# Kernel tuning notes

Hardware: AMD Instinct MI355X
Metric: run time of the kernel (lower is better)

## Reference

```python
import jax, jax.numpy as jnp
import numpy as np
import math

D_MODEL = 512
NHEAD = 8
N_LAYERS = 3
D_FF = 2048
INPUT_DIM = 128
NUM_CLASSES = 64
FACTOR = 5


def setup_inputs() -> dict:
    key = jax.random.key(0)
    ks = jax.random.split(key, 24)
    s = 0.02
    d, f, nl = D_MODEL, D_FF, N_LAYERS
    inp = {
        "x": jax.random.normal(ks[0], (4, 1024, INPUT_DIM), dtype=jnp.float32),
        "W_emb": jax.random.normal(ks[1], (INPUT_DIM, d), dtype=jnp.float32) * s,
        "b_emb": jnp.zeros((d,), jnp.float32),
        "Wq": jax.random.normal(ks[2], (nl, d, d), dtype=jnp.float32) * s,
        "bq": jnp.zeros((nl, d), jnp.float32),
        "Wk": jax.random.normal(ks[3], (nl, d, d), dtype=jnp.float32) * s,
        "bk": jnp.zeros((nl, d), jnp.float32),
        "Wv": jax.random.normal(ks[4], (nl, d, d), dtype=jnp.float32) * s,
        "bv": jnp.zeros((nl, d), jnp.float32),
        "Wo": jax.random.normal(ks[5], (nl, d, d), dtype=jnp.float32) * s,
        "bo": jnp.zeros((nl, d), jnp.float32),
        "ln1_g": jnp.ones((nl, d), jnp.float32),
        "ln1_b": jnp.zeros((nl, d), jnp.float32),
        "W1": jax.random.normal(ks[6], (nl, d, f), dtype=jnp.float32) * s,
        "b1": jnp.zeros((nl, f), jnp.float32),
        "W2": jax.random.normal(ks[7], (nl, f, d), dtype=jnp.float32) * s,
        "b2": jnp.zeros((nl, d), jnp.float32),
        "ln2_g": jnp.ones((nl, d), jnp.float32),
        "ln2_b": jnp.zeros((nl, d), jnp.float32),
        "W_dec": jax.random.normal(ks[8], (d, NUM_CLASSES), dtype=jnp.float32) * s,
        "b_dec": jnp.zeros((NUM_CLASSES,), jnp.float32),
    }
    return inp


def _layer_norm(x, g, b, eps=1e-5):
    m = jnp.mean(x, axis=-1, keepdims=True)
    v = jnp.var(x, axis=-1, keepdims=True)
    return (x - m) * jax.lax.rsqrt(v + eps) * g + b


def _pos_encoding(L, d):
    pos = jnp.arange(L, dtype=jnp.float32)[:, None]
    div = jnp.exp(jnp.arange(0, d, 2, dtype=jnp.float32) * (-math.log(10000.0) / d))
    pe = jnp.zeros((L, d), jnp.float32)
    pe = pe.at[:, 0::2].set(jnp.sin(pos * div))
    pe = pe.at[:, 1::2].set(jnp.cos(pos * div))
    return pe


def _prob_sparse_attn(x, Wq, bq, Wk, bk, Wv, bv, Wo, bo):
    B, L, d = x.shape
    H, dk = NHEAD, d // NHEAD
    u = min(L, int(FACTOR * math.log(L)) if L > 1 else L)
    Q = (x @ Wq + bq).reshape(B, L, H, dk).transpose(0, 2, 1, 3)  # bhld
    K = (x @ Wk + bk).reshape(B, L, H, dk).transpose(0, 2, 1, 3)
    V = (x @ Wv + bv).reshape(B, L, H, dk).transpose(0, 2, 1, 3)
    scores = jnp.einsum("bhld,bhmd->bhlm", Q, K) / math.sqrt(dk)  # [B,H,L,L]
    kth = jax.lax.top_k(scores, u)[0][..., -1:]  # kth-largest per row
    scores = jnp.where(scores < kth, -10000.0, scores)
    attn = jax.nn.softmax(scores, axis=-1)
    out = jnp.einsum("bhlm,bhmd->bhld", attn, V)
    out = out.transpose(0, 2, 1, 3).reshape(B, L, d)
    return out @ Wo + bo


def reference(x, W_emb, b_emb, Wq, bq, Wk, bk, Wv, bv, Wo, bo,
              ln1_g, ln1_b, W1, b1, W2, b2, ln2_g, ln2_b, W_dec, b_dec):
    B, L, _ = x.shape
    h = (x @ W_emb + b_emb) * math.sqrt(D_MODEL)
    h = h + _pos_encoding(L, D_MODEL)[None]
    for i in range(N_LAYERS):
        a = _prob_sparse_attn(h, Wq[i], bq[i], Wk[i], bk[i], Wv[i], bv[i], Wo[i], bo[i])
        h = _layer_norm(h + a, ln1_g[i], ln1_b[i])
        ff = jax.nn.relu(h @ W1[i] + b1[i]) @ W2[i] + b2[i]
        h = _layer_norm(h + ff, ln2_g[i], ln2_b[i])
    return h @ W_dec + b_dec
```

## Files before the change

kernel.cpp:

```cpp
#include <hip/hip_runtime.h>
#include <math.h>

#define SEQ 1024
#define BATCH 4
#define DMODEL 512
#define NHEAD 8
#define DK 64
#define DFF 2048
#define U_TOP 34
#define ROWS (BATCH * SEQ)

typedef unsigned short ushort_t;
typedef __attribute__((ext_vector_type(8))) short short8;
typedef __attribute__((ext_vector_type(4))) float float4v;

__device__ inline ushort_t f2bf(float f) {
  unsigned u = __float_as_uint(f);
  unsigned r = u + 0x7fffu + ((u >> 16) & 1u);
  return (ushort_t)(r >> 16);
}
__device__ inline float bf2f(ushort_t u) {
  return __uint_as_float((unsigned)u << 16);
}
__device__ inline float keyinv(unsigned cand) {
  unsigned fb = (cand & 0x80000000u) ? (cand ^ 0x80000000u) : ~cand;
  return __uint_as_float(fb);
}

__device__ inline void glds16(const void* g, void* l) {
  __builtin_amdgcn_global_load_lds(
      (const __attribute__((address_space(1))) unsigned int*)g,
      (__attribute__((address_space(3))) unsigned int*)l, 16, 0, 0);
}

__device__ inline float bitonic64_desc(float sv, int lane) {
#pragma unroll
  for (int k = 2; k <= 64; k <<= 1) {
#pragma unroll
    for (int j = k >> 1; j > 0; j >>= 1) {
      float pv = __shfl_xor(sv, j);
      bool keepMin = (((lane & k) != 0) == ((lane & j) == 0));
      sv = keepMin ? fminf(sv, pv) : fmaxf(sv, pv);
    }
  }
  return sv;
}

template <int RELU, int SPLIT>
__global__ __launch_bounds__(256) void gemm128(
    const ushort_t* __restrict__ A, const short* __restrict__ Bt,
    const float* __restrict__ b0, const float* __restrict__ b1,
    const float* __restrict__ b2, ushort_t* __restrict__ Cout,
    int K, int N, int zCstride) {
  __shared__ short As[128 * 32];
  __shared__ short Bs[128 * 32];

  const int tid = threadIdx.x;
  const int lane = tid & 63, w = tid >> 6;
  const int wm = w >> 1, wn = w & 1;
  const int quad = lane >> 4, r16 = lane & 15;
  const int bm = blockIdx.y * 128, bn = blockIdx.x * 128;

  const int srow = lane >> 2, skseg = lane & 3;
  const ushort_t* Ag0 = A + (size_t)(bm + w * 16 + srow) * K + skseg * 8;
  const ushort_t* Ag1 = Ag0 + (size_t)64 * K;
  const short* Bg0 = Bt + (size_t)(bn + w * 16 + srow) * K + skseg * 8;
  const short* Bg1 = Bg0 + (size_t)64 * K;
  short* lA0 = As + (w * 16) * 32;
  short* lA1 = As + (64 + w * 16) * 32;
  short* lB0 = Bs + (w * 16) * 32;
  short* lB1 = Bs + (64 + w * 16) * 32;

  float4v acc[4][4];
#pragma unroll
  for (int m = 0; m < 4; ++m)
#pragma unroll
    for (int n = 0; n < 4; ++n) acc[m][n] = (float4v){0.f, 0.f, 0.f, 0.f};

  for (int k0 = 0; k0 < K; k0 += 32) {
    __syncthreads();
    glds16(Ag0 + k0, lA0);
    glds16(Ag1 + k0, lA1);
    glds16(Bg0 + k0, lB0);
    glds16(Bg1 + k0, lB1);
    __syncthreads();

    short8 af[4], bfr[4];
#pragma unroll
    for (int m = 0; m < 4; ++m)
      af[m] = *(const short8*)&As[(wm * 64 + m * 16 + r16) * 32 + quad * 8];
#pragma unroll
    for (int n = 0; n < 4; ++n)
      bfr[n] = *(const short8*)&Bs[(wn * 64 + n * 16 + r16) * 32 + quad * 8];
#pragma unroll
    for (int m = 0; m < 4; ++m)
#pragma unroll
      for (int n = 0; n < 4; ++n)
        acc[m][n] = __builtin_amdgcn_mfma_f32_16x16x32_bf16(af[m], bfr[n],
                                                            acc[m][n], 0, 0, 0);
  }

  const int z = SPLIT ? (bn >> 9) : 0;
  const float* bias = (z == 0) ? b0 : (z == 1 ? b1 : b2);
  const int cbase = SPLIT ? (bn & 511) : bn;
  const int strideN = SPLIT ? 512 : N;
  ushort_t* C = Cout + (SPLIT ? (size_t)z * zCstride : (size_t)0);

  float bias_n[4];
#pragma unroll
  for (int n = 0; n < 4; ++n)
    bias_n[n] = bias[cbase + wn * 64 + n * 16 + r16];

#pragma unroll
  for (int m = 0; m < 4; ++m) {
#pragma unroll
    for (int n = 0; n < 4; ++n) {
      int col = cbase + wn * 64 + n * 16 + r16;
#pragma unroll
      for (int reg = 0; reg < 4; ++reg) {
        int row = bm + wm * 64 + m * 16 + quad * 4 + reg;
        float v = acc[m][n][reg] + bias_n[n];
        if (RELU) v = fmaxf(v, 0.f);
        C[(size_t)row * strideN + col] = f2bf(v);
      }
    }
  }
}

template <int RELU, int OUTBF16, int EPI, int ADDC>
__global__ __launch_bounds__(256) void gemm64(
    const ushort_t* __restrict__ A, const short* __restrict__ Bt,
    const float* __restrict__ bias, void* __restrict__ Cout,
    const ushort_t* __restrict__ Cadd, int K, int N) {
  __shared__ short As[64 * 32];
  __shared__ short Bs[64 * 32];

  const int tid = threadIdx.x;
  const int lane = tid & 63, w = tid >> 6;
  const int wm = w >> 1, wn = w & 1;
  const int quad = lane >> 4, r16 = lane & 15;
  const int bm = blockIdx.y * 64, bn = blockIdx.x * 64;

  const int srow = tid >> 2, skseg = tid & 3;
  const ushort_t* Ag = A + (size_t)(bm + srow) * K + skseg * 8;
  const short* Bg = Bt + (size_t)(bn + srow) * K + skseg * 8;
  short* lA = As + w * 512;
  short* lB = Bs + w * 512;

  float4v acc[2][2];
#pragma unroll
  for (int m = 0; m < 2; ++m)
#pragma unroll
    for (int n = 0; n < 2; ++n) acc[m][n] = (float4v){0.f, 0.f, 0.f, 0.f};

  for (int k0 = 0; k0 < K; k0 += 32) {
    __syncthreads();
    glds16(Ag + k0, lA);
    glds16(Bg + k0, lB);
    __syncthreads();

    short8 af[2], bfr[2];
#pragma unroll
    for (int m = 0; m < 2; ++m)
      af[m] = *(const short8*)&As[(wm * 32 + m * 16 + r16) * 32 + quad * 8];
#pragma unroll
    for (int n = 0; n < 2; ++n)
      bfr[n] = *(const short8*)&Bs[(wn * 32 + n * 16 + r16) * 32 + quad * 8];
#pragma unroll
    for (int m = 0; m < 2; ++m)
#pragma unroll
      for (int n = 0; n < 2; ++n)
        acc[m][n] = __builtin_amdgcn_mfma_f32_16x16x32_bf16(af[m], bfr[n],
                                                            acc[m][n], 0, 0, 0);
  }

  const float pe_c = (float)(-9.210340371976184 / 512.0);
  const float sqrtd = 22.62741699796952f;

  float bias_n[2];
#pragma unroll
  for (int n = 0; n < 2; ++n) bias_n[n] = bias[bn + wn * 32 + n * 16 + r16];

#pragma unroll
  for (int m = 0; m < 2; ++m) {
#pragma unroll
    for (int n = 0; n < 2; ++n) {
      int col = bn + wn * 32 + n * 16 + r16;
#pragma unroll
      for (int reg = 0; reg < 4; ++reg) {
        int row = bm + wm * 32 + m * 16 + quad * 4 + reg;
        float v = acc[m][n][reg] + bias_n[n];
        if (RELU) v = fmaxf(v, 0.f);
        if (EPI == 2) {
          int pos = row & (SEQ - 1);
          float e = __expf((float)(col & ~1) * pe_c);
          float arg = (float)pos * e;
          v = v * sqrtd + ((col & 1) ? __cosf(arg) : __sinf(arg));
        }
        if (ADDC) v += bf2f(Cadd[(size_t)row * N + col]);
        if (OUTBF16) {
          ((ushort_t*)Cout)[(size_t)row * N + col] = f2bf(v);
        } else {
          ((float*)Cout)[(size_t)row * N + col] = v;
        }
      }
    }
  }
}

__global__ __launch_bounds__(256) void convert_all(
    const float* __restrict__ Wq, const float* __restrict__ Wk,
    const float* __restrict__ Wv, const float* __restrict__ Wo,
    const float* __restrict__ W1, const float* __restrict__ W2,
    const float* __restrict__ W_emb, const float* __restrict__ W_dec,
    short* __restrict__ wt) {
  __shared__ float t[32][33];
  int id = blockIdx.x;
  const float* src;
  short* dst;
  int K, N, tk, tn;
  if (id < 9216) {
    int lay = id / 3072, r = id % 3072;
    short* wl = wt + (size_t)lay * 3145728;
    const size_t wsz = 512 * 512;
    if (r < 1024) {
      int wi = r >> 8, tile = r & 255;
      const float* base = (wi == 0) ? Wq : (wi == 1) ? Wk : (wi == 2) ? Wv : Wo;
      src = base + lay * wsz;
      dst = wl + wi * 262144;
      K = 512; N = 512; tk = tile >> 4; tn = tile & 15;
    } else if (r < 2048) {
      int tile = r - 1024;
      src = W1 + (size_t)lay * 512 * 2048;
      dst = wl + 1048576;
      K = 512; N = 2048; tk = tile >> 6; tn = tile & 63;
    } else {
      int tile = r - 2048;
      src = W2 + (size_t)lay * 2048 * 512;
      dst = wl + 2097152;
      K = 2048; N = 512; tk = tile >> 4; tn = tile & 15;
    }
  } else {
    int r = id - 9216;
    if (r < 64) {
      src = W_emb; dst = wt + 9437184; K = 128; N = 512; tk = r >> 4; tn = r & 15;
    } else {
      r -= 64;
      src = W_dec; dst = wt + 9502720; K = 512; N = 64; tk = r >> 1; tn = r & 1;
    }
  }
  const int k0 = tk * 32, n0 = tn * 32;
  const int tx = threadIdx.x, ty = threadIdx.y;
#pragma unroll
  for (int i = 0; i < 4; ++i) {
    int r = ty + i * 8;
    t[r][tx] = src[(size_t)(k0 + r) * N + n0 + tx];
  }
  __syncthreads();
#pragma unroll
  for (int i = 0; i < 4; ++i) {
    int r = ty + i * 8;
    dst[(size_t)(n0 + r) * K + k0 + tx] = (short)f2bf(t[tx][r]);
  }
}

__global__ __launch_bounds__(256) void f32_to_bf16_kernel(
    const float* __restrict__ src, ushort_t* __restrict__ dst) {
  int i = blockIdx.x * blockDim.x + threadIdx.x;
  float4 v = ((const float4*)src)[i];
  ushort4 o;
  o.x = f2bf(v.x); o.y = f2bf(v.y); o.z = f2bf(v.z); o.w = f2bf(v.w);
  ((ushort4*)dst)[i] = o;
}

__global__ __launch_bounds__(256) void ln_kernel(
    const ushort_t* __restrict__ t1b, const float* __restrict__ g,
    const float* __restrict__ bb, ushort_t* __restrict__ hb) {
  const int row = blockIdx.x * 4 + (threadIdx.x >> 6);
  const int lane = threadIdx.x & 63;
  const size_t base = (size_t)row * DMODEL + lane * 8;
  uint4 raw = *(const uint4*)(t1b + base);
  unsigned rr[4] = {raw.x, raw.y, raw.z, raw.w};
  float v[8];
#pragma unroll
  for (int k = 0; k < 4; ++k) {
    v[2 * k] = bf2f((ushort_t)(rr[k] & 0xffff));
    v[2 * k + 1] = bf2f((ushort_t)(rr[k] >> 16));
  }
  float sum = 0.f, sq = 0.f;
#pragma unroll
  for (int k = 0; k < 8; ++k) { sum += v[k]; sq += v[k] * v[k]; }
#pragma unroll
  for (int off = 32; off; off >>= 1) {
    sum += __shfl_xor(sum, off);
    sq += __shfl_xor(sq, off);
  }
  float mean = sum * (1.f / 512.f);
  float var = fmaxf(sq * (1.f / 512.f) - mean * mean, 0.f);
  float rstd = 1.f / sqrtf(var + 1e-5f);
  float4 g0 = *(const float4*)(g + lane * 8);
  float4 g1 = *(const float4*)(g + lane * 8 + 4);
  float4 c0 = *(const float4*)(bb + lane * 8);
  float4 c1 = *(const float4*)(bb + lane * 8 + 4);
  float gg[8] = {g0.x, g0.y, g0.z, g0.w, g1.x, g1.y, g1.z, g1.w};
  float cc[8] = {c0.x, c0.y, c0.z, c0.w, c1.x, c1.y, c1.z, c1.w};
  uint4 out;
  unsigned* op = (unsigned*)&out;
#pragma unroll
  for (int k = 0; k < 4; ++k) {
    float y0 = (v[2 * k] - mean) * rstd * gg[2 * k] + cc[2 * k];
    float y1 = (v[2 * k + 1] - mean) * rstd * gg[2 * k + 1] + cc[2 * k + 1];
    op[k] = (unsigned)f2bf(y0) | ((unsigned)f2bf(y1) << 16);
  }
  *(uint4*)(hb + base) = out;
}

#define SSTR 1028

__global__ __launch_bounds__(1024, 8) void attn_kernel(
    const ushort_t* __restrict__ Qb, const ushort_t* __restrict__ Kb,
    const ushort_t* __restrict__ Vb, ushort_t* __restrict__ Ob) {
  __shared__ float s[16 * SSTR];
  __shared__ int jlist[16][64];
  __shared__ float wlist[16][64];

  const int tid = threadIdx.x;
  const int q0 = blockIdx.x * 16;
  const int h = blockIdx.y;
  const int b = blockIdx.z;
  const int w = tid >> 6;
  const int lane = tid & 63;
  const int quad = lane >> 4, r16 = lane & 15;

  {
    const int j0 = w * 64;
    const ushort_t* qrow =
        Qb + (size_t)(b * SEQ + q0 + r16) * DMODEL + h * DK + quad * 8;
    short8 aq0 = *(const short8*)qrow;
    short8 aq1 = *(const short8*)(qrow + 32);

    float4v acc[4];
#pragma unroll
    for (int nt = 0; nt < 4; ++nt) {
      const ushort_t* krow =
          Kb + (size_t)(b * SEQ + j0 + nt * 16 + r16) * DMODEL + h * DK +
          quad * 8;
      short8 bk0 = *(const short8*)krow;
      short8 bk1 = *(const short8*)(krow + 32);
      float4v a = (float4v){0.f, 0.f, 0.f, 0.f};
      a = __builtin_amdgcn_mfma_f32_16x16x32_bf16(aq0, bk0, a, 0, 0, 0);
      a = __builtin_amdgcn_mfma_f32_16x16x32_bf16(aq1, bk1, a, 0, 0, 0);
      acc[nt] = a;
    }
#pragma unroll
    for (int nt = 0; nt < 4; ++nt)
#pragma unroll
      for (int reg = 0; reg < 4; ++reg)
        s[(quad * 4 + reg) * SSTR + j0 + nt * 16 + r16] =
            acc[nt][reg] * 0.125f;
  }
  __syncthreads();

  {
    float v[16];
    float lmax = -1e30f;
#pragma unroll
    for (int i = 0; i < 16; ++i) {
      float f = s[w * SSTR + lane + 64 * i];
      v[i] = f;
      lmax = fmaxf(lmax, f);
    }

    float srt = bitonic64_desc(lmax, lane);
    const float mx = __shfl(srt, 0);
    const float fT = __shfl(srt, 33);

    const unsigned long long lmask_lt = (1ull << lane) - 1ull;
    float* tmpv = &wlist[w][0];
    int* tmpj = &jlist[w][0];

    int basec = 0;
#pragma unroll
    for (int i = 0; i < 16; ++i) {
      bool gk = v[i] >= fT;
      unsigned long long mask = __ballot(gk);
      if (gk) {
        int p = basec + (int)__popcll(mask & lmask_lt);
        if (p < 64) { tmpv[p] = v[i]; tmpj[p] = lane + 64 * i; }
      }
      basec += (int)__popcll(mask);
    }
    int ncand = basec;
    if (basec > 64) {
      unsigned ans = 0u;
      int cge = basec, bit = 31;
      bool ex = false;
      while (bit >= 0 && cge > 64 && !ex) {
        unsigned cand = ans | (1u << bit);
        float fc = keyinv(cand);
        int c = 0;
#pragma unroll
        for (int i = 0; i < 16; ++i) c += (int)__popcll(__ballot(v[i] >= fc));
        if (c >= U_TOP) { ans = cand; cge = c; ex = (c == U_TOP); }
        --bit;
      }
      float fa = keyinv(ans);
      int b2 = 0;
#pragma unroll
      for (int i = 0; i < 16; ++i) {
        bool gk = v[i] >= fa;
        unsigned long long mask = __ballot(gk);
        if (gk) {
          int p = b2 + (int)__popcll(mask & lmask_lt);
          if (p < 64) { tmpv[p] = v[i]; tmpj[p] = lane + 64 * i; }
        }
        b2 += (int)__popcll(mask);
      }
      ncand = b2 > 64 ? 64 : b2;
    }

    float cf = (lane < ncand) ? tmpv[lane] : -3.4e38f;
    int cj = (lane < ncand) ? tmpj[lane] : 0;

    float srt2 = bitonic64_desc(cf, lane);
    const float thr = __shfl(srt2, 33);

    bool keep = cf >= thr;
    unsigned long long kmask = __ballot(keep);
    int n = (int)__popcll(kmask);
    float e = keep ? __expf(cf - mx) : 0.f;
    float zsum = e;
#pragma unroll
    for (int off = 32; off; off >>= 1) zsum += __shfl_xor(zsum, off);
    int pos = (int)__popcll(kmask & lmask_lt);
    if (keep) { jlist[w][pos] = cj; wlist[w][pos] = e; }

    const ushort_t* vbase = Vb + (size_t)b * SEQ * DMODEL + h * DK;
    float o = 0.f;
    int i = 0;
    for (; i + 4 <= n; i += 4) {
      int j0 = jlist[w][i], j1 = jlist[w][i + 1];
      int j2 = jlist[w][i + 2], j3 = jlist[w][i + 3];
      float w0 = wlist[w][i], w1 = wlist[w][i + 1];
      float w2 = wlist[w][i + 2], w3 = wlist[w][i + 3];
      float p0 = bf2f(vbase[(size_t)j0 * DMODEL + lane]);
      float p1 = bf2f(vbase[(size_t)j1 * DMODEL + lane]);
      float p2 = bf2f(vbase[(size_t)j2 * DMODEL + lane]);
      float p3 = bf2f(vbase[(size_t)j3 * DMODEL + lane]);
      o += w0 * p0 + w1 * p1 + w2 * p2 + w3 * p3;
    }
    for (; i < n; ++i)
      o += wlist[w][i] * bf2f(vbase[(size_t)jlist[w][i] * DMODEL + lane]);
    o /= zsum;
    Ob[(size_t)(b * SEQ + q0 + w) * DMODEL + h * DK + lane] = f2bf(o);
  }
}

extern "C" void kernel_launch(void* const* d_in, const int* in_sizes, int n_in,
                              void* d_out, int out_size, void* d_ws,
                              size_t ws_size, hipStream_t stream) {
  const float* x = (const float*)d_in[0];
  const float* W_emb = (const float*)d_in[1];
  const float* b_emb = (const float*)d_in[2];
  const float* Wq = (const float*)d_in[3];
  const float* bq = (const float*)d_in[4];
  const float* Wk = (const float*)d_in[5];
  const float* bk = (const float*)d_in[6];
  const float* Wv = (const float*)d_in[7];
  const float* bv = (const float*)d_in[8];
  const float* Wo = (const float*)d_in[9];
  const float* bo = (const float*)d_in[10];
  const float* ln1_g = (const float*)d_in[11];
  const float* ln1_b = (const float*)d_in[12];
  const float* W1 = (const float*)d_in[13];
  const float* b1 = (const float*)d_in[14];
  const float* W2 = (const float*)d_in[15];
  const float* b2 = (const float*)d_in[16];
  const float* ln2_g = (const float*)d_in[17];
  const float* ln2_b = (const float*)d_in[18];
  const float* W_dec = (const float*)d_in[19];
  const float* b_dec = (const float*)d_in[20];

  char* wsb = (char*)d_ws;
  ushort_t* qkv = (ushort_t*)wsb;
  ushort_t* ffh = (ushort_t*)wsb;
  ushort_t* ao = (ushort_t*)(wsb + ((size_t)16 << 20));
  ushort_t* xb = (ushort_t*)(wsb + ((size_t)16 << 20));
  ushort_t* t1b = (ushort_t*)(wsb + ((size_t)20 << 20));
  ushort_t* hb = (ushort_t*)(wsb + ((size_t)24 << 20));
  short* wt = (short*)(wsb + ((size_t)28 << 20));
  short* wembT = wt + 9437184;
  short* wdecT = wt + 9502720;

  f32_to_bf16_kernel<<<dim3(512), 256, 0, stream>>>(x, xb);
  convert_all<<<dim3(9312), dim3(32, 8), 0, stream>>>(Wq, Wk, Wv, Wo, W1, W2,
                                                      W_emb, W_dec, wt);
  gemm64<0, 1, 2, 0><<<dim3(8, 64), 256, 0, stream>>>(
      xb, wembT, b_emb, (void*)hb, nullptr, 128, 512);

  for (int i = 0; i < 3; ++i) {
    short* wtL = wt + (size_t)i * 3145728;

    gemm128<0, 1><<<dim3(12, 32), 256, 0, stream>>>(
        hb, wtL, bq + i * DMODEL, bk + i * DMODEL, bv + i * DMODEL, qkv, 512,
        512, 2097152);

    attn_kernel<<<dim3(SEQ / 16, NHEAD, BATCH), dim3(1024), 0, stream>>>(
        qkv, qkv + 2097152, qkv + 4194304, ao);

    gemm64<0, 1, 0, 1><<<dim3(8, 64), 256, 0, stream>>>(
        ao, wtL + 786432, bo + i * DMODEL, (void*)t1b, hb, 512, 512);
    ln_kernel<<<dim3(ROWS / 4), 256, 0, stream>>>(
        t1b, ln1_g + i * DMODEL, ln1_b + i * DMODEL, hb);

    gemm128<1, 0><<<dim3(16, 32), 256, 0, stream>>>(
        hb, wtL + 1048576, b1 + i * DFF, nullptr, nullptr, ffh, 512, 2048, 0);
    gemm64<0, 1, 0, 1><<<dim3(8, 64), 256, 0, stream>>>(
        ffh, wtL + 2097152, b2 + i * DMODEL, (void*)t1b, hb, 2048, 512);
    ln_kernel<<<dim3(ROWS / 4), 256, 0, stream>>>(
        t1b, ln2_g + i * DMODEL, ln2_b + i * DMODEL, hb);
  }

  gemm64<0, 0, 0, 0><<<dim3(1, 64), 256, 0, stream>>>(
      hb, wdecT, b_dec, d_out, nullptr, 512, 64);
}
```

Baseline: 557.3 us.

## Halve attention block size, store scores in fp16, process two rows per wave

The attention kernel now runs 512 threads per block, and each wave handles two query rows at once with interleaved bitonic sorts and ballots. The score matrix in shared memory moves from fp32 to fp16, and index plus exp weight are packed into one 32-bit list entry, which cuts LDS footprint. Exponentials are computed during candidate selection, and the V gather loop is interleaved across the two rows to expose more memory parallelism. This risks precision loss from fp16 scores and weights, and the top-k threshold choice can change when scores tie after rounding.

Result: no change. 564.0 us (+1.2%).

```diff
diff --git a/kernel.cpp b/kernel.cpp
--- a/kernel.cpp
+++ b/kernel.cpp
@@ -27,23 +27,36 @@
   return __uint_as_float(fb);
 }
 
+union H16 { _Float16 h; unsigned short u; };
+__device__ inline unsigned short h2u(float f) {
+  H16 t; t.h = (_Float16)f; return t.u;
+}
+__device__ inline float u2h(unsigned short u) {
+  H16 t; t.u = u; return (float)t.h;
+}
+__device__ inline int mbcnt64(unsigned long long m) {
+  int lo = __builtin_amdgcn_mbcnt_lo((unsigned)m, 0);
+  return __builtin_amdgcn_mbcnt_hi((unsigned)(m >> 32), lo);
+}
+
 __device__ inline void glds16(const void* g, void* l) {
   __builtin_amdgcn_global_load_lds(
       (const __attribute__((address_space(1))) unsigned int*)g,
       (__attribute__((address_space(3))) unsigned int*)l, 16, 0, 0);
 }
 
-__device__ inline float bitonic64_desc(float sv, int lane) {
+__device__ inline void bitonic64x2(float& a, float& b, int lane) {
 #pragma unroll
   for (int k = 2; k <= 64; k <<= 1) {
 #pragma unroll
     for (int j = k >> 1; j > 0; j >>= 1) {
-      float pv = __shfl_xor(sv, j);
+      float pa = __shfl_xor(a, j);
+      float pb = __shfl_xor(b, j);
       bool keepMin = (((lane & k) != 0) == ((lane & j) == 0));
-      sv = keepMin ? fminf(sv, pv) : fmaxf(sv, pv);
-    }
-  }
-  return sv;
+      a = keepMin ? fminf(a, pa) : fmaxf(a, pa);
+      b = keepMin ? fminf(b, pb) : fmaxf(b, pb);
+    }
+  }
 }
 
 template <int RELU, int SPLIT>
@@ -315,14 +328,13 @@
   *(uint4*)(hb + base) = out;
 }
 
-#define SSTR 1028
-
-__global__ __launch_bounds__(1024, 8) void attn_kernel(
+#define SST 1048
+
+__global__ __launch_bounds__(512, 8) void attn_kernel(
     const ushort_t* __restrict__ Qb, const ushort_t* __restrict__ Kb,
     const ushort_t* __restrict__ Vb, ushort_t* __restrict__ Ob) {
-  __shared__ float s[16 * SSTR];
-  __shared__ int jlist[16][64];
-  __shared__ float wlist[16][64];
+  __shared__ _Float16 s16[16 * SST];
+  __shared__ unsigned plist[16][64];
 
   const int tid = threadIdx.x;
   const int q0 = blockIdx.x * 16;
@@ -333,15 +345,14 @@
   const int quad = lane >> 4, r16 = lane & 15;
 
   {
-    const int j0 = w * 64;
+    const int j0 = w * 128;
     const ushort_t* qrow =
         Qb + (size_t)(b * SEQ + q0 + r16) * DMODEL + h * DK + quad * 8;
     short8 aq0 = *(const short8*)qrow;
     short8 aq1 = *(const short8*)(qrow + 32);
 
-    float4v acc[4];
-#pragma unroll
-    for (int nt = 0; nt < 4; ++nt) {
+#pragma unroll
+    for (int nt = 0; nt < 8; ++nt) {
       const ushort_t* krow =
           Kb + (size_t)(b * SEQ + j0 + nt * 16 + r16) * DMODEL + h * DK +
           quad * 8;
@@ -350,109 +361,162 @@
       float4v a = (float4v){0.f, 0.f, 0.f, 0.f};
       a = __builtin_amdgcn_mfma_f32_16x16x32_bf16(aq0, bk0, a, 0, 0, 0);
       a = __builtin_amdgcn_mfma_f32_16x16x32_bf16(aq1, bk1, a, 0, 0, 0);
-      acc[nt] = a;
-    }
-#pragma unroll
-    for (int nt = 0; nt < 4; ++nt)
 #pragma unroll
       for (int reg = 0; reg < 4; ++reg)
-        s[(quad * 4 + reg) * SSTR + j0 + nt * 16 + r16] =
-            acc[nt][reg] * 0.125f;
+        s16[(quad * 4 + reg) * SST + j0 + nt * 16 + r16] =
+            (_Float16)(a[reg] * 0.125f);
+    }
   }
   __syncthreads();
 
   {
-    float v[16];
-    float lmax = -1e30f;
+    const int qa = w, qb2 = w + 8;
+    const _Float16* sa = &s16[qa * SST];
+    const _Float16* sb = &s16[qb2 * SST];
+
+    float la = -1e30f, lb = -1e30f;
 #pragma unroll
     for (int i = 0; i < 16; ++i) {
-      float f = s[w * SSTR + lane + 64 * i];
-      v[i] = f;
-      lmax = fmaxf(lmax, f);
-    }
-
-    float srt = bitonic64_desc(lmax, lane);
-    const float mx = __shfl(srt, 0);
-    const float fT = __shfl(srt, 33);
-
-    const unsigned long long lmask_lt = (1ull << lane) - 1ull;
-    float* tmpv = &wlist[w][0];
-    int* tmpj = &jlist[w][0];
-
-    int basec = 0;
+      la = fmaxf(la, (float)sa[lane + 64 * i]);
+      lb = fmaxf(lb, (float)sb[lane + 64 * i]);
+    }
+
+    float sva = la, svb = lb;
+    bitonic64x2(sva, svb, lane);
+    const float mxa = __shfl(sva, 0), mxb = __shfl(svb, 0);
+    const float fTa = __shfl(sva, 33), fTb = __shfl(svb, 33);
+
+    int ca = 0, cb = 0;
 #pragma unroll
     for (int i = 0; i < 16; ++i) {
-      bool gk = v[i] >= fT;
-      unsigned long long mask = __ballot(gk);
-      if (gk) {
-        int p = basec + (int)__popcll(mask & lmask_lt);
-        if (p < 64) { tmpv[p] = v[i]; tmpj[p] = lane + 64 * i; }
-      }
-      basec += (int)__popcll(mask);
-    }
-    int ncand = basec;
-    if (basec > 64) {
+      float va = (float)sa[lane + 64 * i];
+      float vb = (float)sb[lane + 64 * i];
+      bool ka = va >= fTa, kb = vb >= fTb;
+      unsigned long long ma = __ballot(ka);
+      unsigned long long mb = __ballot(kb);
+      if (ka) {
+        int p = ca + mbcnt64(ma);
+        if (p < 64)
+          plist[qa][p] = ((unsigned)(lane + 64 * i) << 16) |
+                         h2u(__expf(va - mxa));
+      }
+      if (kb) {
+        int p = cb + mbcnt64(mb);
+        if (p < 64)
+          plist[qb2][p] = ((unsigned)(lane + 64 * i) << 16) |
+                          h2u(__expf(vb - mxb));
+      }
+      ca += (int)__popcll(ma);
+      cb += (int)__popcll(mb);
+    }
+
+    if (__builtin_expect(ca > 64, 0)) {
       unsigned ans = 0u;
-      int cge = basec, bit = 31;
+      int cge = ca;
       bool ex = false;
-      while (bit >= 0 && cge > 64 && !ex) {
+      for (int bit = 31; bit >= 0 && cge > 64 && !ex; --bit) {
         unsigned cand = ans | (1u << bit);
         float fc = keyinv(cand);
         int c = 0;
 #pragma unroll
-        for (int i = 0; i < 16; ++i) c += (int)__popcll(__ballot(v[i] >= fc));
+        for (int i = 0; i < 16; ++i)
+          c += (int)__popcll(__ballot((float)sa[lane + 64 * i] >= fc));
         if (c >= U_TOP) { ans = cand; cge = c; ex = (c == U_TOP); }
-        --bit;
-      }
-      float fa = keyinv(ans);
-      int b2 = 0;
+      }
+      float fa2 = keyinv(ans);
+      int cc = 0;
 #pragma unroll
       for (int i = 0; i < 16; ++i) {
-        bool gk = v[i] >= fa;
-        unsigned long long mask = __ballot(gk);
-        if (gk) {
-          int p = b2 + (int)__popcll(mask & lmask_lt);
-          if (p < 64) { tmpv[p] = v[i]; tmpj[p] = lane + 64 * i; }
+        float va = (float)sa[lane + 64 * i];
+        bool ka = va >= fa2;
+        unsigned long long ma = __ballot(ka);
+        if (ka) {
+          int p = cc + mbcnt64(ma);
+          if (p < 64)
+            plist[qa][p] = ((unsigned)(lane + 64 * i) << 16) |
+                           h2u(__expf(va - mxa));
         }
-        b2 += (int)__popcll(mask);
-      }
-      ncand = b2 > 64 ? 64 : b2;
-    }
-
-    float cf = (lane < ncand) ? tmpv[lane] : -3.4e38f;
-    int cj = (lane < ncand) ? tmpj[lane] : 0;
-
-    float srt2 = bitonic64_desc(cf, lane);
-    const float thr = __shfl(srt2, 33);
-
-    bool keep = cf >= thr;
-    unsigned long long kmask = __ballot(keep);
-    int n = (int)__popcll(kmask);
-    float e = keep ? __expf(cf - mx) : 0.f;
-    float zsum = e;
-#pragma unroll
-    for (int off = 32; off; off >>= 1) zsum += __shfl_xor(zsum, off);
-    int pos = (int)__popcll(kmask & lmask_lt);
-    if (keep) { jlist[w][pos] = cj; wlist[w][pos] = e; }
+        cc += (int)__popcll(ma);
+      }
+      ca = cc;
+    }
+    if (__builtin_expect(cb > 64, 0)) {
+      unsigned ans = 0u;
+      int cge = cb;
+      bool ex = false;
+      for (int bit = 31; bit >= 0 && cge > 64 && !ex; --bit) {
+        unsigned cand = ans | (1u << bit);
+        float fc = keyinv(cand);
+        int c = 0;
+#pragma unroll
+        for (int i = 0; i < 16; ++i)
+          c += (int)__popcll(__ballot((float)sb[lane + 64 * i] >= fc));
+        if (c >= U_TOP) { ans = cand; cge = c; ex = (c == U_TOP); }
+      }
+      float fb2 = keyinv(ans);
+      int cc = 0;
+#pragma unroll
+      for (int i = 0; i < 16; ++i) {
+        float vb = (float)sb[lane + 64 * i];
+        bool kb = vb >= fb2;
+        unsigned long long mb = __ballot(kb);
+        if (kb) {
+          int p = cc + mbcnt64(mb);
+          if (p < 64)
+            plist[qb2][p] = ((unsigned)(lane + 64 * i) << 16) |
+                            h2u(__expf(vb - mxb));
+        }
+        cc += (int)__popcll(mb);
+      }
+      cb = cc;
+    }
+    ca = ca > 64 ? 64 : ca;
+    cb = cb > 64 ? 64 : cb;
+
+    unsigned pua = (lane < ca) ? plist[qa][lane] : 0u;
+    unsigned pub = (lane < cb) ? plist[qb2][lane] : 0u;
+    float ea = u2h((unsigned short)(pua & 0xffffu));
+    float eb = u2h((unsigned short)(pub & 0xffffu));
+
+    float s2a = ea, s2b = eb;
+    bitonic64x2(s2a, s2b, lane);
+    const float tha = __shfl(s2a, 33), thb = __shfl(s2b, 33);
+
+    bool keepa = ea >= tha, keepb = eb >= thb;
+    unsigned long long kma = __ballot(keepa);
+    unsigned long long kmb = __ballot(keepb);
+    int na = (int)__popcll(kma), nb = (int)__popcll(kmb);
+    float za = keepa ? ea : 0.f, zb = keepb ? eb : 0.f;
+#pragma unroll
+    for (int off = 32; off; off >>= 1) {
+      za += __shfl_xor(za, off);
+      zb += __shfl_xor(zb, off);
+    }
+    int posa = mbcnt64(kma), posb = mbcnt64(kmb);
+    if (keepa) plist[qa][posa] = pua;
+    if (keepb) plist[qb2][posb] = pub;
 
     const ushort_t* vbase = Vb + (size_t)b * SEQ * DMODEL + h * DK;
-    float o = 0.f;
-    int i = 0;
-    for (; i + 4 <= n; i += 4) {
-      int j0 = jlist[w][i], j1 = jlist[w][i + 1];
-      int j2 = jlist[w][i + 2], j3 = jlist[w][i + 3];
-      float w0 = wlist[w][i], w1 = wlist[w][i + 1];
-      float w2 = wlist[w][i + 2], w3 = wlist[w][i + 3];
-      float p0 = bf2f(vbase[(size_t)j0 * DMODEL + lane]);
-      float p1 = bf2f(vbase[(size_t)j1 * DMODEL + lane]);
-      float p2 = bf2f(vbase[(size_t)j2 * DMODEL + lane]);
-      float p3 = bf2f(vbase[(size_t)j3 * DMODEL + lane]);
-      o += w0 * p0 + w1 * p1 + w2 * p2 + w3 * p3;
-    }
-    for (; i < n; ++i)
-      o += wlist[w][i] * bf2f(vbase[(size_t)jlist[w][i] * DMODEL + lane]);
-    o /= zsum;
-    Ob[(size_t)(b * SEQ + q0 + w) * DMODEL + h * DK + lane] = f2bf(o);
+    float oa = 0.f, ob = 0.f;
+    int nmax = na > nb ? na : nb;
+    for (int i = 0; i < nmax; i += 2) {
+      unsigned ua0 = (i < na) ? plist[qa][i] : 0u;
+      unsigned ua1 = (i + 1 < na) ? plist[qa][i + 1] : 0u;
+      unsigned ub0 = (i < nb) ? plist[qb2][i] : 0u;
+      unsigned ub1 = (i + 1 < nb) ? plist[qb2][i + 1] : 0u;
+      float pa0 = bf2f(vbase[(size_t)(ua0 >> 16) * DMODEL + lane]);
+      float pa1 = bf2f(vbase[(size_t)(ua1 >> 16) * DMODEL + lane]);
+      float pb0 = bf2f(vbase[(size_t)(ub0 >> 16) * DMODEL + lane]);
+      float pb1 = bf2f(vbase[(size_t)(ub1 >> 16) * DMODEL + lane]);
+      oa += u2h((unsigned short)(ua0 & 0xffffu)) * pa0 +
+            u2h((unsigned short)(ua1 & 0xffffu)) * pa1;
+      ob += u2h((unsigned short)(ub0 & 0xffffu)) * pb0 +
+            u2h((unsigned short)(ub1 & 0xffffu)) * pb1;
+    }
+    oa /= za;
+    ob /= zb;
+    Ob[(size_t)(b * SEQ + q0 + qa) * DMODEL + h * DK + lane] = f2bf(oa);
+    Ob[(size_t)(b * SEQ + q0 + qb2) * DMODEL + h * DK + lane] = f2bf(ob);
   }
 }
 
@@ -505,7 +569,7 @@
         hb, wtL, bq + i * DMODEL, bk + i * DMODEL, bv + i * DMODEL, qkv, 512,
         512, 2097152);
 
-    attn_kernel<<<dim3(SEQ / 16, NHEAD, BATCH), dim3(1024), 0, stream>>>(
+    attn_kernel<<<dim3(SEQ / 16, NHEAD, BATCH), dim3(512), 0, stream>>>(
         qkv, qkv + 2097152, qkv + 4194304, ao);
 
     gemm64<0, 1, 0, 1><<<dim3(8, 64), 256, 0, stream>>>(
```
